# Kernel optimization log

Hardware: AMD Instinct MI355X
Metric: run time of the kernel (lower is better)

Reference implementation:

```python
import jax, jax.numpy as jnp
import numpy as np

N_WIRES = 8
DIM = 2 ** N_WIRES  # 256
N_OPS = 20

# Fixed realization of tq.RandomLayer(n_ops=20): ops drawn once with a fixed seed.
_rs = np.random.RandomState(0)
RAND_OPS = []
for _ in range(N_OPS):
    k = int(_rs.randint(4))
    if k == 3:
        c, t = _rs.choice(N_WIRES, 2, replace=False)
        RAND_OPS.append(("cnot", int(c), int(t)))
    else:
        RAND_OPS.append((("rx", "ry", "rz")[k], int(_rs.randint(N_WIRES)), 0))

_idx = np.arange(DIM)
# Z eigenvalue sign per wire per basis state (wire 0 = most significant bit)
ZSIGN_NP = np.stack([1.0 - 2.0 * ((_idx >> (N_WIRES - 1 - w)) & 1) for w in range(N_WIRES)]).astype(np.float32)
ZSIGN = jnp.asarray(ZSIGN_NP)        # [8, 256]
ZS_T = jnp.asarray(ZSIGN_NP.T)       # [256, 8]

# CNOT is a basis permutation: precompute index maps for each cnot op.
PERMS = {}
for _i, _op in enumerate(RAND_OPS):
    if _op[0] == "cnot":
        _c, _t = _op[1], _op[2]
        _cb = (_idx >> (N_WIRES - 1 - _c)) & 1
        PERMS[_i] = jnp.asarray(_idx ^ (_cb << (N_WIRES - 1 - _t)))


def _ry_mat(t):
    c = jnp.cos(t * 0.5).astype(jnp.complex64)
    s = jnp.sin(t * 0.5).astype(jnp.complex64)
    return jnp.stack([jnp.stack([c, -s]), jnp.stack([s, c])])


def _rx_mat(t):
    c = jnp.cos(t * 0.5).astype(jnp.complex64)
    s = (-1j * jnp.sin(t * 0.5)).astype(jnp.complex64)
    return jnp.stack([jnp.stack([c, s]), jnp.stack([s, c])])


def _apply_1q(state, U, w):
    # state: [B, 256]; apply 2x2 U on wire w
    B = state.shape[0]
    s = state.reshape(B, 2 ** w, 2, -1)
    return jnp.einsum('ij,bajc->baic', U, s).reshape(B, DIM)


def _forward(x, ry_theta, rand_params, W1, b1, W2, b2):
    B, S, E = x.shape
    f = x.reshape(B * S, E)[:, :N_WIRES]  # encoder uses input_idx 0..7
    # Encoder: RY(f_w) on |0> for each wire -> product state, built by kron chain
    c = jnp.cos(f * 0.5)
    s = jnp.sin(f * 0.5)
    state = jnp.ones((B * S, 1), jnp.float32)
    for w in range(N_WIRES):
        v = jnp.stack([c[:, w], s[:, w]], axis=-1)  # [BS, 2]
        state = (state[:, :, None] * v[:, None, :]).reshape(B * S, -1)
    state = state.astype(jnp.complex64)  # [BS, 256]
    # Fixed random layer
    for i, op in enumerate(RAND_OPS):
        kind = op[0]
        if kind == "cnot":
            state = state[:, PERMS[i]]
        elif kind == "rz":
            ph = jnp.exp((-0.5j * rand_params[i]) * ZSIGN[op[1]]).astype(jnp.complex64)
            state = state * ph[None, :]
        elif kind == "rx":
            state = _apply_1q(state, _rx_mat(rand_params[i]), op[1])
        else:
            state = _apply_1q(state, _ry_mat(rand_params[i]), op[1])
    # Trainable per-wire RY gates
    for w in range(N_WIRES):
        state = _apply_1q(state, _ry_mat(ry_theta[w]), w)
    # MeasureAll(PauliZ): <Z_w> = sum_b |amp_b|^2 * zsign_w(b)
    probs = (state.real ** 2 + state.imag ** 2)  # [BS, 256] float32
    expv = probs @ ZS_T                          # [BS, 8]
    h = jax.nn.relu(expv @ W1.T + b1)
    out = h @ W2.T + b2
    return out.reshape(B, S, -1)


def setup_inputs() -> dict:
    key = jax.random.key(0)
    k1, k2, k3, k4, k5 = jax.random.split(key, 5)
    B, S, E = 4, 4096, 512
    pi = 3.14159265
    x = jax.random.normal(k1, (B, S, E), jnp.float32)
    ry_theta = jax.random.uniform(k2, (N_WIRES,), jnp.float32, -pi, pi)
    rand_params = jax.random.uniform(k3, (N_OPS,), jnp.float32, -pi, pi)
    W1 = jax.random.normal(k4, (64, N_WIRES), jnp.float32) * (1.0 / np.sqrt(N_WIRES))
    b1 = jnp.zeros((64,), jnp.float32)
    W2 = jax.random.normal(k5, (E, 64), jnp.float32) * (1.0 / 8.0)
    b2 = jnp.zeros((E,), jnp.float32)
    return {"x": x, "ry_theta": ry_theta, "rand_params": rand_params, "W1": W1, "b1": b1, "W2": W2, "b2": b2}


def reference(x, ry_theta, rand_params, W1, b1, W2, b2):
    return _forward(x, ry_theta, rand_params, W1, b1, W2, b2)
```

## Files before the change

### kernel.cpp

```cpp
#include <hip/hip_runtime.h>
#include <hip/hip_fp16.h>
#include <cstdint>

#define N_RAND   20
#define N_GATES  28
#define E_DIM    512

struct OpsArg { int d[N_GATES]; };

struct MT19937ce {
  uint32_t mt[624] = {};
  int mti = 0;
  constexpr void seed(uint32_t s){
    mt[0]=s;
    for(int i=1;i<624;i++) mt[i]=1812433253u*(mt[i-1]^(mt[i-1]>>30))+(uint32_t)i;
    mti=624;
  }
  constexpr uint32_t next(){
    if(mti>=624){
      for(int i=0;i<624;i++){
        uint32_t y=(mt[i]&0x80000000u)|(mt[(i+1)%624]&0x7fffffffu);
        mt[i]=mt[(i+397)%624]^(y>>1)^((y&1u)?0x9908b0dfu:0u);
      }
      mti=0;
    }
    uint32_t y=mt[mti++];
    y^=y>>11; y^=(y<<7)&0x9d2c5680u; y^=(y<<15)&0xefc60000u; y^=y>>18;
    return y;
  }
  constexpr uint32_t interval(uint32_t mx){
    if(!mx) return 0;
    uint32_t mask=mx; mask|=mask>>1; mask|=mask>>2; mask|=mask>>4; mask|=mask>>8; mask|=mask>>16;
    uint32_t v = next()&mask;
    while(v>mx) v = next()&mask;
    return v;
  }
};

constexpr OpsArg build_ops_ce(){
  MT19937ce rs; rs.seed(0);
  OpsArg o{};
  for(int i=0;i<N_RAND;i++){
    uint32_t k = rs.interval(3);
    if(k==3){
      int perm[8] = {0,1,2,3,4,5,6,7};
      for(int j=7;j>=1;j--){
        uint32_t t=rs.interval((uint32_t)j);
        int tmp=perm[j]; perm[j]=perm[t]; perm[t]=tmp;
      }
      o.d[i] = 3 | (perm[0]<<2) | (perm[1]<<5);
    } else {
      uint32_t w = rs.interval(7);
      o.d[i] = (int)k | ((int)w<<2);
    }
  }
  for(int i=0;i<8;i++) o.d[N_RAND+i] = 1 | (i<<2);
  return o;
}
inline constexpr OpsArg OPS = build_ops_ce();

__device__ __forceinline__ float readlane_f(float v, int l){
  return __int_as_float(__builtin_amdgcn_readlane(__float_as_int(v), l));
}
template<int CTRL>
__device__ __forceinline__ float dpp_mov(float v){
  int s = __float_as_int(v);
  return __int_as_float(__builtin_amdgcn_update_dpp(s, s, CTRL, 0xF, 0xF, false));
}
template<int M>
__device__ __forceinline__ float xl(float v){
  if constexpr (M==1)      return dpp_mov<0xB1>(v);
  else if constexpr (M==2) return dpp_mov<0x4E>(v);
  else return __int_as_float(__builtin_amdgcn_ds_swizzle(__float_as_int(v), (M<<10)|0x1F));
}
template<int L>
__device__ __forceinline__ float bcast(float v){
  return __int_as_float(__builtin_amdgcn_ds_swizzle(__float_as_int(v), L<<5));
}

typedef _Float16 v2h __attribute__((ext_vector_type(2)));
typedef _Float16 v8h __attribute__((ext_vector_type(8)));
typedef float    v4f __attribute__((ext_vector_type(4)));
union HU { uint32_t u; v2h h; };

template<int G>
__device__ __forceinline__ void run_gates(float (&ar)[8], float (&ai)[8],
                                          const float (&sgn)[5], int l,
                                          float cv, float sv)
{
  if constexpr (G < N_GATES){
    constexpr int dd   = OPS.d[G];
    constexpr int kind = dd & 3;
    constexpr int wa   = (dd>>2) & 7;
    constexpr int wb   = (dd>>5) & 7;
    const float gc = readlane_f(cv, G);
    const float gs = readlane_f(sv, G);

    if constexpr (kind == 3){
      if constexpr (wa < 3 && wb < 3){
        constexpr int Rc = 4>>wa, Rt = 4>>wb;
        #pragma unroll
        for (int r=0;r<8;r++){
          if ((r & Rc) && !(r & Rt)){
            float t0=ar[r]; ar[r]=ar[r|Rt]; ar[r|Rt]=t0;
            float t1=ai[r]; ai[r]=ai[r|Rt]; ai[r|Rt]=t1;
          }
        }
      } else if constexpr (wa < 3){
        constexpr int Rc = 4>>wa, Mt = 16>>(wb-3);
        #pragma unroll
        for (int r=0;r<8;r++){
          if (r & Rc){ ar[r]=xl<Mt>(ar[r]); ai[r]=xl<Mt>(ai[r]); }
        }
      } else if constexpr (wb < 3){
        constexpr int Mc = 16>>(wa-3), Rt = 4>>wb;
        const bool cb = (l & Mc) != 0;
        #pragma unroll
        for (int r=0;r<8;r++){
          if (!(r & Rt)){
            float alo=ar[r], ahi=ar[r|Rt];
            ar[r]    = cb ? ahi : alo;  ar[r|Rt] = cb ? alo : ahi;
            float blo=ai[r], bhi=ai[r|Rt];
            ai[r]    = cb ? bhi : blo;  ai[r|Rt] = cb ? blo : bhi;
          }
        }
      } else {
        constexpr int Mc = 16>>(wa-3), Mt = 16>>(wb-3);
        const bool cb = (l & Mc) != 0;
        #pragma unroll
        for (int r=0;r<8;r++){
          float pr = xl<Mt>(ar[r]), pi_ = xl<Mt>(ai[r]);
          ar[r] = cb ? pr  : ar[r];
          ai[r] = cb ? pi_ : ai[r];
        }
      }
    } else if constexpr (kind == 2){
      if constexpr (wa < 3){
        constexpr int Rb = 4>>wa;
        #pragma unroll
        for (int r=0;r<8;r++){
          const float pim = (r & Rb) ? gs : -gs;
          float nr = gc*ar[r] - pim*ai[r];
          ai[r] = gc*ai[r] + pim*ar[r];
          ar[r] = nr;
        }
      } else {
        constexpr int SI = wa-3;
        const float pim = sgn[SI]*gs;
        #pragma unroll
        for (int r=0;r<8;r++){
          float nr = gc*ar[r] - pim*ai[r];
          ai[r] = gc*ai[r] + pim*ar[r];
          ar[r] = nr;
        }
      }
    } else if constexpr (kind == 1){
      if constexpr (wa < 3){
        constexpr int Rb = 4>>wa;
        #pragma unroll
        for (int r=0;r<8;r++){
          if (!(r & Rb)){
            const int h = r|Rb;
            float lr=ar[r], li=ai[r], hr=ar[h], hii=ai[h];
            ar[r]=gc*lr - gs*hr;  ai[r]=gc*li - gs*hii;
            ar[h]=gs*lr + gc*hr;  ai[h]=gs*li + gc*hii;
          }
        }
      } else {
        constexpr int M = 16>>(wa-3), SI = wa-3;
        const float sg = sgn[SI]*gs;
        #pragma unroll
        for (int r=0;r<8;r++){
          float pr = xl<M>(ar[r]), pi_ = xl<M>(ai[r]);
          ar[r] = gc*ar[r] + sg*pr;
          ai[r] = gc*ai[r] + sg*pi_;
        }
      }
    } else {
      if constexpr (wa < 3){
        constexpr int Rb = 4>>wa;
        #pragma unroll
        for (int r=0;r<8;r++){
          if (!(r & Rb)){
            const int h = r|Rb;
            float lr=ar[r], li=ai[r], hr=ar[h], hii=ai[h];
            ar[r]=gc*lr + gs*hii;  ai[r]=gc*li - gs*hr;
            ar[h]=gc*hr + gs*li;   ai[h]=gc*hii - gs*lr;
          }
        }
      } else {
        constexpr int M = 16>>(wa-3);
        #pragma unroll
        for (int r=0;r<8;r++){
          float pr = xl<M>(ar[r]), pi_ = xl<M>(ai[r]);
          ar[r] = gc*ar[r] + gs*pi_;
          ai[r] = gc*ai[r] - gs*pr;
        }
      }
    }
    run_gates<G+1>(ar, ai, sgn, l, cv, sv);
  }
}

__global__ __launch_bounds__(256)
void qcirc_kernel(const float* __restrict__ x,
                  const float* __restrict__ ry_theta,
                  const float* __restrict__ rand_params,
                  const float* __restrict__ W1,
                  const float* __restrict__ b1,
                  __half* __restrict__ Hout)
{
  const int tid  = threadIdx.x;
  const int lane = tid & 63;
  const int l    = lane & 31;
  const int wave = tid >> 6;
  const int token = blockIdx.x*8 + wave*2 + (lane>>5);

  float th = 0.f;
  if (lane < N_GATES)
    th = (lane < N_RAND) ? rand_params[lane] : ry_theta[lane - N_RAND];
  float cv, sv;
  __sincosf(0.5f*th, &sv, &cv);

  const float4 xa = *(const float4*)(x + (size_t)token*E_DIM);
  const float4 xb = *(const float4*)(x + (size_t)token*E_DIM + 4);
  float c[8], s[8];
  {
    float xs[8] = {xa.x, xa.y, xa.z, xa.w, xb.x, xb.y, xb.z, xb.w};
    #pragma unroll
    for (int w=0; w<8; ++w) __sincosf(0.5f*xs[w], &s[w], &c[w]);
  }

  float sgn[5];
  sgn[0] = (l&16) ? 1.f : -1.f;
  sgn[1] = (l& 8) ? 1.f : -1.f;
  sgn[2] = (l& 4) ? 1.f : -1.f;
  sgn[3] = (l& 2) ? 1.f : -1.f;
  sgn[4] = (l& 1) ? 1.f : -1.f;

  float lp = ((l&16)? s[3]:c[3]) * ((l&8)? s[4]:c[4]);
  lp *= ((l&4)? s[5]:c[5]) * ((l&2)? s[6]:c[6]);
  lp *= ((l&1)? s[7]:c[7]);
  const float q00=c[0]*c[1], q01=c[0]*s[1], q10=s[0]*c[1], q11=s[0]*s[1];
  const float c2lp=c[2]*lp, s2lp=s[2]*lp;
  float ar[8], ai[8];
  ar[0]=q00*c2lp; ar[1]=q00*s2lp; ar[2]=q01*c2lp; ar[3]=q01*s2lp;
  ar[4]=q10*c2lp; ar[5]=q10*s2lp; ar[6]=q11*c2lp; ar[7]=q11*s2lp;
  #pragma unroll
  for (int r=0;r<8;r++) ai[r]=0.f;

  run_gates<0>(ar, ai, sgn, l, cv, sv);

  float p[8];
  #pragma unroll
  for (int r=0;r<8;r++) p[r] = ar[r]*ar[r] + ai[r]*ai[r];
  const float t1a=p[0]+p[1], t1b=p[2]+p[3], t1c=p[4]+p[5], t1d=p[6]+p[7];
  const float s0a=t1a+t1b, s0b=t1c+t1d;
  float P  = s0a + s0b;
  float e0 = s0a - s0b;
  float e1 = (t1a+t1c) - (t1b+t1d);
  float e2 = (p[0]-p[1])+(p[2]-p[3])+(p[4]-p[5])+(p[6]-p[7]);

  {
    float t;
    t=xl<1>(e0); e0+=t;  t=xl<1>(e1); e1+=t;  t=xl<1>(e2); e2+=t;
    t=xl<1>(P);  P = fmaf(-sgn[4], P, t);
    t=xl<2>(e0); e0+=t;  t=xl<2>(e1); e1+=t;  t=xl<2>(e2); e2+=t;
    t=xl<2>(P);  P = fmaf(-sgn[3], P, t);
    t=xl<4>(e0); e0+=t;  t=xl<4>(e1); e1+=t;  t=xl<4>(e2); e2+=t;
    t=xl<4>(P);  P = fmaf(-sgn[2], P, t);
    t=xl<8>(e0); e0+=t;  t=xl<8>(e1); e1+=t;  t=xl<8>(e2); e2+=t;
    t=xl<8>(P);  P = fmaf(-sgn[1], P, t);
    t=xl<16>(e0); e0+=t; t=xl<16>(e1); e1+=t; t=xl<16>(e2); e2+=t;
    t=xl<16>(P); P = fmaf(-sgn[0], P, t);
  }
  const float e3 = bcast<16>(P);
  const float e4 = bcast<8>(P);
  const float e5 = bcast<4>(P);
  const float e6 = bcast<2>(P);
  const float e7 = bcast<1>(P);

  const float4 wA0 = *(const float4*)(W1 + (size_t)(2*l)*8);
  const float4 wA1 = *(const float4*)(W1 + (size_t)(2*l)*8 + 4);
  const float4 wB0 = *(const float4*)(W1 + (size_t)(2*l+1)*8);
  const float4 wB1 = *(const float4*)(W1 + (size_t)(2*l+1)*8 + 4);
  const float2 bb  = *(const float2*)(b1 + 2*l);
  float h0 = bb.x + wA0.x*e0 + wA0.y*e1 + wA0.z*e2 + wA0.w*e3
                  + wA1.x*e4 + wA1.y*e5 + wA1.z*e6 + wA1.w*e7;
  float h1 = bb.y + wB0.x*e0 + wB0.y*e1 + wB0.z*e2 + wB0.w*e3
                  + wB1.x*e4 + wB1.y*e5 + wB1.z*e6 + wB1.w*e7;
  HU pk;
  pk.h = v2h{(_Float16)fmaxf(h0,0.f), (_Float16)fmaxf(h1,0.f)};
  *(uint32_t*)((char*)Hout + ((size_t)token*64 + 2*l)*2) = pk.u;
}

__global__ __launch_bounds__(256)
void w2cvt_kernel(const float* __restrict__ W2, __half* __restrict__ W2h)
{
  const int i = blockIdx.x*256 + threadIdx.x;
  const float4 v = *(const float4*)(W2 + (size_t)i*4);
  HU a, b;
  a.h = v2h{(_Float16)v.x, (_Float16)v.y};
  b.h = v2h{(_Float16)v.z, (_Float16)v.w};
  uint2 o; o.x = a.u; o.y = b.u;
  *(uint2*)((char*)W2h + (size_t)i*8) = o;
}

__global__ __launch_bounds__(256)
void mlp2_mfma(const __half* __restrict__ Hh,
               const __half* __restrict__ W2h,
               const float* __restrict__ b2,
               float* __restrict__ out)
{
  const int tid  = threadIdx.x;
  const int lane = tid & 63;
  const int wid  = blockIdx.x*4 + (tid>>6);
  const int mt   = wid >> 5;
  const int nt   = wid & 31;
  const int rr   = lane & 15;
  const int quad = lane >> 4;

  const v8h a0 = *(const v8h*)(Hh  + ((size_t)(mt*16 + rr))*64 + quad*8);
  const v8h a1 = *(const v8h*)(Hh  + ((size_t)(mt*16 + rr))*64 + 32 + quad*8);
  const v8h b0 = *(const v8h*)(W2h + ((size_t)(nt*16 + rr))*64 + quad*8);
  const v8h b1 = *(const v8h*)(W2h + ((size_t)(nt*16 + rr))*64 + 32 + quad*8);

  v4f acc = {0.f, 0.f, 0.f, 0.f};
  acc = __builtin_amdgcn_mfma_f32_16x16x32_f16(a0, b0, acc, 0, 0, 0);
  acc = __builtin_amdgcn_mfma_f32_16x16x32_f16(a1, b1, acc, 0, 0, 0);

  const float bias = b2[nt*16 + rr];
  #pragma unroll
  for (int r2=0;r2<4;r2++){
    const int t = mt*16 + quad*4 + r2;
    out[(size_t)t*E_DIM + nt*16 + rr] = acc[r2] + bias;
  }
}

extern "C" void kernel_launch(void* const* d_in, const int* in_sizes, int n_in,
                              void* d_out, int out_size, void* d_ws, size_t ws_size,
                              hipStream_t stream)
{
  (void)n_in; (void)out_size; (void)ws_size;
  const int ntok = in_sizes[0] / E_DIM;
  __half* Hh  = (__half*)d_ws;
  __half* W2h = (__half*)((char*)d_ws + (size_t)ntok*64*2);

  w2cvt_kernel<<<(E_DIM*64)/(256*4), 256, 0, stream>>>(
      (const float*)d_in[5], W2h);

  qcirc_kernel<<<ntok/8, 256, 0, stream>>>(
      (const float*)d_in[0],
      (const float*)d_in[1],
      (const float*)d_in[2],
      (const float*)d_in[3],
      (const float*)d_in[4],
      Hh);

  mlp2_mfma<<<(ntok/16)*32/4, 256, 0, stream>>>(
      Hh, W2h,
      (const float*)d_in[6],
      (float*)d_out);
}
```

Baseline: 121.7 us.

## Fuse W2 fp16 conversion into MLP kernel and stage outputs through LDS

Removes the separate W2 conversion kernel launch by loading fp32 W2 directly and converting to fp16 inside the MLP kernel. Each wave now computes four 16x16 output tiles (64 columns) and reuses its H fragments across them. Results are staged in padded shared memory so the output is written as coalesced float4 rows instead of scattered scalar stores. The cost is redundant W2 conversion per wave and an added block barrier.

```diff
diff --git a/kernel.cpp b/kernel.cpp
--- a/kernel.cpp
+++ b/kernel.cpp
@@ -81,7 +81,7 @@
 typedef _Float16 v2h __attribute__((ext_vector_type(2)));
 typedef _Float16 v8h __attribute__((ext_vector_type(8)));
 typedef float    v4f __attribute__((ext_vector_type(4)));
-union HU { uint32_t u; v2h h; };
+union HU  { uint32_t u; v2h h; };
 
 template<int G>
 __device__ __forceinline__ void run_gates(float (&ar)[8], float (&ai)[8],
@@ -260,7 +260,6 @@
   float e0 = s0a - s0b;
   float e1 = (t1a+t1c) - (t1b+t1d);
   float e2 = (p[0]-p[1])+(p[2]-p[3])+(p[4]-p[5])+(p[6]-p[7]);
-
   {
     float t;
     t=xl<1>(e0); e0+=t;  t=xl<1>(e1); e1+=t;  t=xl<1>(e2); e2+=t;
@@ -294,46 +293,56 @@
   *(uint32_t*)((char*)Hout + ((size_t)token*64 + 2*l)*2) = pk.u;
 }
 
+#define TS_STRIDE 68
 __global__ __launch_bounds__(256)
-void w2cvt_kernel(const float* __restrict__ W2, __half* __restrict__ W2h)
+void mlp2_mfma4(const __half* __restrict__ Hh,
+                const float* __restrict__ W2,
+                const float* __restrict__ b2,
+                float* __restrict__ out)
 {
-  const int i = blockIdx.x*256 + threadIdx.x;
-  const float4 v = *(const float4*)(W2 + (size_t)i*4);
-  HU a, b;
-  a.h = v2h{(_Float16)v.x, (_Float16)v.y};
-  b.h = v2h{(_Float16)v.z, (_Float16)v.w};
-  uint2 o; o.x = a.u; o.y = b.u;
-  *(uint2*)((char*)W2h + (size_t)i*8) = o;
-}
-
-__global__ __launch_bounds__(256)
-void mlp2_mfma(const __half* __restrict__ Hh,
-               const __half* __restrict__ W2h,
-               const float* __restrict__ b2,
-               float* __restrict__ out)
-{
+  __shared__ float Ts[4][16*TS_STRIDE];
+
   const int tid  = threadIdx.x;
   const int lane = tid & 63;
-  const int wid  = blockIdx.x*4 + (tid>>6);
-  const int mt   = wid >> 5;
-  const int nt   = wid & 31;
+  const int wave = tid >> 6;
+  const int wid  = blockIdx.x*4 + wave;
+  const int mt   = wid >> 3;
+  const int ng   = wid & 7;
   const int rr   = lane & 15;
   const int quad = lane >> 4;
 
-  const v8h a0 = *(const v8h*)(Hh  + ((size_t)(mt*16 + rr))*64 + quad*8);
-  const v8h a1 = *(const v8h*)(Hh  + ((size_t)(mt*16 + rr))*64 + 32 + quad*8);
-  const v8h b0 = *(const v8h*)(W2h + ((size_t)(nt*16 + rr))*64 + quad*8);
-  const v8h b1 = *(const v8h*)(W2h + ((size_t)(nt*16 + rr))*64 + 32 + quad*8);
-
-  v4f acc = {0.f, 0.f, 0.f, 0.f};
-  acc = __builtin_amdgcn_mfma_f32_16x16x32_f16(a0, b0, acc, 0, 0, 0);
-  acc = __builtin_amdgcn_mfma_f32_16x16x32_f16(a1, b1, acc, 0, 0, 0);
-
-  const float bias = b2[nt*16 + rr];
+  const v8h a0 = *(const v8h*)(Hh + ((size_t)(mt*16 + rr))*64 + quad*8);
+  const v8h a1 = *(const v8h*)(Hh + ((size_t)(mt*16 + rr))*64 + 32 + quad*8);
+
   #pragma unroll
-  for (int r2=0;r2<4;r2++){
-    const int t = mt*16 + quad*4 + r2;
-    out[(size_t)t*E_DIM + nt*16 + rr] = acc[r2] + bias;
+  for (int j=0;j<4;++j){
+    const int e = ng*64 + j*16 + rr;
+    const float4 wa = *(const float4*)(W2 + (size_t)e*64 + quad*8);
+    const float4 wb = *(const float4*)(W2 + (size_t)e*64 + quad*8 + 4);
+    const float4 wc = *(const float4*)(W2 + (size_t)e*64 + 32 + quad*8);
+    const float4 wd = *(const float4*)(W2 + (size_t)e*64 + 32 + quad*8 + 4);
+    const v8h b0 = v8h{(_Float16)wa.x,(_Float16)wa.y,(_Float16)wa.z,(_Float16)wa.w,
+                      (_Float16)wb.x,(_Float16)wb.y,(_Float16)wb.z,(_Float16)wb.w};
+    const v8h b1 = v8h{(_Float16)wc.x,(_Float16)wc.y,(_Float16)wc.z,(_Float16)wc.w,
+                      (_Float16)wd.x,(_Float16)wd.y,(_Float16)wd.z,(_Float16)wd.w};
+    v4f acc = {0.f,0.f,0.f,0.f};
+    acc = __builtin_amdgcn_mfma_f32_16x16x32_f16(a0, b0, acc, 0, 0, 0);
+    acc = __builtin_amdgcn_mfma_f32_16x16x32_f16(a1, b1, acc, 0, 0, 0);
+    #pragma unroll
+    for (int r2=0;r2<4;r2++)
+      Ts[wave][(quad*4+r2)*TS_STRIDE + j*16 + rr] = acc[r2];
+  }
+
+  __syncthreads();
+
+  const float4 bias = *(const float4*)(b2 + ng*64 + rr*4);
+  #pragma unroll
+  for (int k=0;k<4;++k){
+    const int row = 4*k + quad;
+    float4 v = *(const float4*)&Ts[wave][row*TS_STRIDE + rr*4];
+    v.x += bias.x; v.y += bias.y; v.z += bias.z; v.w += bias.w;
+    const int t = mt*16 + row;
+    *(float4*)(out + (size_t)t*E_DIM + ng*64 + rr*4) = v;
   }
 }
 
@@ -343,11 +352,7 @@
 {
   (void)n_in; (void)out_size; (void)ws_size;
   const int ntok = in_sizes[0] / E_DIM;
-  __half* Hh  = (__half*)d_ws;
-  __half* W2h = (__half*)((char*)d_ws + (size_t)ntok*64*2);
-
-  w2cvt_kernel<<<(E_DIM*64)/(256*4), 256, 0, stream>>>(
-      (const float*)d_in[5], W2h);
+  __half* Hh = (__half*)d_ws;
 
   qcirc_kernel<<<ntok/8, 256, 0, stream>>>(
       (const float*)d_in[0],
@@ -357,8 +362,9 @@
       (const float*)d_in[4],
       Hh);
 
-  mlp2_mfma<<<(ntok/16)*32/4, 256, 0, stream>>>(
-      Hh, W2h,
+  mlp2_mfma4<<<(ntok/16)*8/4, 256, 0, stream>>>(
+      Hh,
+      (const float*)d_in[5],
       (const float*)d_in[6],
       (float*)d_out);
 }
```

Measured after the change: 122.0 us, median of 2. Within noise of the previous version (+0.2%).
